# Kernel optimization log

Measured on AMD Instinct MI355X. Metric: run time of the kernel, lower is better.

Reference implementation:

```python
import jax, jax.numpy as jnp
import numpy as np

B, F, D, A = 1024, 33, 128, 128  # batch, num_fields, embed_dim, attn_size (A must equal gnn dim)

def setup_inputs() -> dict:
    key = jax.random.key(0)
    k1, k2, k3, k4 = jax.random.split(key, 4)
    gnn_feature = jax.random.normal(k1, (B, A), dtype=jnp.float32)
    x = jax.random.normal(k2, (B, F, D), dtype=jnp.float32)
    # attention Linear(embed_dim -> attn_size): weight (A, D), bias (A,)
    lim = 1.0 / np.sqrt(D)
    attn_W = jax.random.uniform(k3, (A, D), minval=-lim, maxval=lim, dtype=jnp.float32)
    attn_b = jax.random.uniform(k4, (A,), minval=-lim, maxval=lim, dtype=jnp.float32)
    return {"gnn_feature": gnn_feature, "x": x, "attn_W": attn_W, "attn_b": attn_b}

def reference(gnn_feature, x, attn_W, attn_b):
    num_fields = x.shape[1]
    row, col = np.triu_indices(num_fields, k=1)  # P = F*(F-1)/2 pairs
    inner = x[:, row] * x[:, col]                # [B, P, D]
    fm = jax.nn.relu(jnp.einsum('bpd,ad->bpa', inner, attn_W) + attn_b)  # [B, P, A]
    # bmm(gnn[b,1,A], fm[b,p,A,1]) -> dot product per pair, softmax over pairs
    scores = jnp.einsum('ba,bpa->bp', gnn_feature, fm)  # [B, P]
    attn = jax.nn.softmax(scores, axis=1)               # [B, P]
    attn_output = jnp.einsum('bp,bpd->bd', attn, inner) * 100.0  # [B, D]
    return jnp.concatenate([gnn_feature, attn_output], axis=1)   # [B, A+D]
```

## Files before the change

kernel.cpp:

```cpp
#include <hip/hip_runtime.h>

#define FN 33
#define DN 128
#define AN 128
#define PN 528
#define XS 136
#define TS 36

typedef __attribute__((ext_vector_type(8))) _Float16 half8;
typedef __attribute__((ext_vector_type(4))) float f32x4;
typedef __attribute__((ext_vector_type(4))) unsigned int u32x4;

__device__ __forceinline__ unsigned int pkrtz(float a, float b) {
  return __builtin_bit_cast(unsigned int, __builtin_amdgcn_cvt_pkrtz(a, b));
}

__device__ __forceinline__ float row_sum16(float v) {
  v += __builtin_bit_cast(float, __builtin_amdgcn_update_dpp(0, __builtin_bit_cast(int, v), 0x128, 0xF, 0xF, false));
  v += __builtin_bit_cast(float, __builtin_amdgcn_update_dpp(0, __builtin_bit_cast(int, v), 0x124, 0xF, 0xF, false));
  v += __builtin_bit_cast(float, __builtin_amdgcn_update_dpp(0, __builtin_bit_cast(int, v), 0x122, 0xF, 0xF, false));
  v += __builtin_bit_cast(float, __builtin_amdgcn_update_dpp(0, __builtin_bit_cast(int, v), 0x121, 0xF, 0xF, false));
  return v;
}

#define XLOAD(XV, XT, BB)                                                     \
  {                                                                           \
    const f32x4* xb = (const f32x4*)(xg + (size_t)(BB) * FN * DN);            \
    _Pragma("unroll")                                                         \
    for (int s = 0; s < 4; s++) {                                             \
      XV[s] = xb[tid + s * 256];                                              \
      asm volatile("" : "+v"(XV[s]));                                         \
    }                                                                         \
    if (tid < 32) XT = xb[1024 + tid];                                        \
    asm volatile("" : "+v"(XT));                                              \
  }

#define XSTORE(XV, XT, BUFI)                                                  \
  {                                                                           \
    _Pragma("unroll")                                                         \
    for (int s = 0; s < 4; s++) {                                             \
      const int idx = tid + s * 256;                                          \
      const int i = idx >> 5, d0 = (idx & 31) << 2;                           \
      *(uint2*)&xh[BUFI][i * XS + d0] =                                       \
          make_uint2(pkrtz(XV[s].x, XV[s].y), pkrtz(XV[s].z, XV[s].w));       \
    }                                                                         \
    if (tid < 32) {                                                           \
      const int idx = 1024 + tid;                                             \
      const int i = idx >> 5, d0 = (idx & 31) << 2;                           \
      *(uint2*)&xh[BUFI][i * XS + d0] =                                       \
          make_uint2(pkrtz(XT.x, XT.y), pkrtz(XT.z, XT.w));                   \
    }                                                                         \
  }

#define WALK(XHB, GB, SPB, RMAXP)                                             \
  {                                                                           \
    const int t_beg = mh ? 17 : 0;                                            \
    const int t_end = mh ? 33 : 17;                                           \
    float wm = -3.4e38f;                                                      \
    unsigned int rc_next = rowcol[t_beg * 16 + u];                            \
    for (int t = t_beg; t < t_end; ++t) {                                     \
      const unsigned int rc = rc_next;                                        \
      if (t + 1 < t_end) rc_next = rowcol[(t + 1) * 16 + u];                  \
      const int r = rc & 255, c = rc >> 8;                                    \
      const _Float16* xr_base = &XHB[r * XS + q * 8];                         \
      const _Float16* xc_base = &XHB[c * XS + q * 8];                         \
      f32x4 acc[4];                                                           \
      _Pragma("unroll")                                                       \
      for (int nn = 0; nn < 4; nn++)                                          \
        acc[nn] = (f32x4){barr[nn], barr[nn], barr[nn], barr[nn]};            \
      __builtin_amdgcn_s_setprio(1);                                          \
      _Pragma("unroll")                                                       \
      for (int kk = 0; kk < 4; kk++) {                                        \
        half8 af = *(const half8*)(xr_base + kk * 32) *                       \
                   *(const half8*)(xc_base + kk * 32);                        \
        _Pragma("unroll")                                                     \
        for (int nn = 0; nn < 4; nn++)                                        \
          acc[nn] = __builtin_amdgcn_mfma_f32_16x16x32_f16(af, Bf[nn][kk],    \
                                                           acc[nn], 0, 0, 0);  \
      }                                                                       \
      __builtin_amdgcn_s_setprio(0);                                          \
      float sc[4] = {0.f, 0.f, 0.f, 0.f};                                     \
      _Pragma("unroll")                                                       \
      for (int nn = 0; nn < 4; nn++)                                          \
        _Pragma("unroll")                                                     \
        for (int rr = 0; rr < 4; rr++)                                        \
          sc[rr] = fmaf(fmaxf(acc[nn][rr], 0.f), GB[nn], sc[rr]);             \
      _Pragma("unroll")                                                       \
      for (int rr = 0; rr < 4; rr++) sc[rr] = row_sum16(sc[rr]);              \
      wm = fmaxf(wm, fmaxf(fmaxf(sc[0], sc[1]), fmaxf(sc[2], sc[3])));        \
      if (u == 0)                                                             \
        *(f32x4*)&SPB[t * 16 + q * 4] = (f32x4){sc[0], sc[1], sc[2], sc[3]};  \
    }                                                                         \
    wm = fmaxf(wm, __shfl_xor(wm, 16, 64));                                   \
    wm = fmaxf(wm, __shfl_xor(wm, 32, 64));                                   \
    if (lane == 0) RMAXP[wave] = wm;                                          \
  }

#define SPH(PARM)                                                             \
  {                                                                           \
    const float Mh = fmaxf(rmax[PARM][0], rmax[PARM][2]) +                    \
                     fmaxf(rmax[PARM][1], rmax[PARM][3]);                     \
    float s0 = sp[PARM][0][tid] + sp[PARM][1][tid];                           \
    float s1 = sp[PARM][0][tid + 256] + sp[PARM][1][tid + 256];               \
    float e0 = __expf(s0 - Mh);                                               \
    float e1 = __expf(s1 - Mh);                                               \
    unsigned int rc = rowcol[tid];                                            \
    attn2d[PARM][(rc & 255) * TS + ((rc >> 8) - (rc & 255) - 1)] = e0;        \
    rc = rowcol[tid + 256];                                                   \
    attn2d[PARM][(rc & 255) * TS + ((rc >> 8) - (rc & 255) - 1)] = e1;        \
    float e2 = 0.f;                                                           \
    if (tid < 16) {                                                           \
      float s2 = sp[PARM][0][tid + 512] + sp[PARM][1][tid + 512];             \
      e2 = __expf(s2 - Mh);                                                   \
      rc = rowcol[tid + 512];                                                 \
      attn2d[PARM][(rc & 255) * TS + ((rc >> 8) - (rc & 255) - 1)] = e2;      \
    }                                                                         \
    float ls = (e0 + e1) + e2;                                                \
    _Pragma("unroll")                                                         \
    for (int off = 32; off >= 1; off >>= 1) ls += __shfl_xor(ls, off, 64);    \
    if (lane == 0) rsum[PARM][wave] = ls;                                     \
  }

#define EPH(PARM, XHB, BB)                                                    \
  if (tid < 128) {                                                            \
    const float Zb = (rsum[PARM][0] + rsum[PARM][1]) +                        \
                     (rsum[PARM][2] + rsum[PARM][3]);                         \
    const int d = tid;                                                        \
    float xcol[36];                                                           \
    _Pragma("unroll")                                                         \
    for (int i = 0; i < FN; i++) xcol[i] = (float)XHB[i * XS + d];            \
    xcol[33] = 0.f; xcol[34] = 0.f; xcol[35] = 0.f;                           \
    float accv = 0.f;                                                         \
    _Pragma("unroll")                                                         \
    for (int i = 0; i < 32; i++) {                                            \
      const int L = FN - 1 - i;                                               \
      const int nf4 = (L + 3) >> 2;                                           \
      float ti = 0.f;                                                         \
      _Pragma("unroll")                                                       \
      for (int t = 0; t < nf4; t++) {                                         \
        f32x4 a4 = *(const f32x4*)&attn2d[PARM][i * TS + t * 4];              \
        ti = fmaf(a4.x, xcol[i + 1 + t * 4 + 0], ti);                         \
        ti = fmaf(a4.y, xcol[i + 1 + t * 4 + 1], ti);                         \
        ti = fmaf(a4.z, xcol[i + 1 + t * 4 + 2], ti);                         \
        ti = fmaf(a4.w, xcol[i + 1 + t * 4 + 3], ti);                         \
      }                                                                       \
      accv = fmaf(xcol[i], ti, accv);                                         \
    }                                                                         \
    out[(size_t)(BB) * (AN + DN) + AN + d] = accv * (100.0f / Zb);            \
  } else {                                                                    \
    const int a = tid - 128;                                                  \
    out[(size_t)(BB) * (AN + DN) + a] = gnn[(size_t)(BB) * AN + a];           \
  }

__global__ __launch_bounds__(256, 2)
void afm_kernel(const float* __restrict__ gnn, const float* __restrict__ xg,
                const float* __restrict__ Wg,  const float* __restrict__ bg,
                float* __restrict__ out)
{
  __shared__ __align__(16) _Float16 xh[2][FN * XS];
  __shared__ __align__(16) float attn2d[2][FN * TS];
  __shared__ __align__(16) float sp[2][2][PN];
  __shared__ unsigned short rowcol[PN];
  __shared__ float rmax[2][4], rsum[2][4];

  const int tid  = threadIdx.x;
  const int b0   = blockIdx.x * 2;
  const int b1   = b0 + 1;
  const int wave = tid >> 6;
  const int lane = tid & 63;
  const int q    = lane >> 4;
  const int u    = lane & 15;
  const int nh   = wave & 1;
  const int mh   = wave >> 1;

  f32x4 xv0[4], xv1[4];
  f32x4 xt0 = {0,0,0,0}, xt1 = {0,0,0,0};
  XLOAD(xv0, xt0, b0);
  XLOAD(xv1, xt1, b1);

  half8 Bf[4][4];
  float g0[4], g1[4], barr[4];
  #pragma unroll
  for (int nn = 0; nn < 4; nn++) {
    const int a = nh * 64 + nn * 16 + u;
    const float* src = Wg + (size_t)a * DN + q * 8;
    #pragma unroll
    for (int kk = 0; kk < 4; kk++) {
      f32x4 w0 = *(const f32x4*)(src + kk * 32);
      f32x4 w1 = *(const f32x4*)(src + kk * 32 + 4);
      u32x4 pk;
      pk.x = pkrtz(w0.x, w0.y);
      pk.y = pkrtz(w0.z, w0.w);
      pk.z = pkrtz(w1.x, w1.y);
      pk.w = pkrtz(w1.z, w1.w);
      Bf[nn][kk] = __builtin_bit_cast(half8, pk);
      asm volatile("" : "+v"(Bf[nn][kk]));
    }
    g0[nn] = gnn[(size_t)b0 * AN + a];
    g1[nn] = gnn[(size_t)b1 * AN + a];
    barr[nn] = bg[a];
    asm volatile("" : "+v"(g0[nn]), "+v"(g1[nn]), "+v"(barr[nn]));
  }

  {
    float* a2z = &attn2d[0][0];
    for (int idx = tid; idx < 2 * FN * TS; idx += 256) a2z[idx] = 0.0f;
    for (int p = tid; p < PN; p += 256) {
      int i = 0, rem = p;
      while (rem >= FN - 1 - i) { rem -= FN - 1 - i; i++; }
      rowcol[p] = (unsigned short)(i | ((i + 1 + rem) << 8));
    }
  }
  XSTORE(xv0, xt0, 0);
  XSTORE(xv1, xt1, 1);
  __syncthreads();

  WALK(xh[0], g0, (&sp[0][nh][0]), rmax[0]);
  __syncthreads();

  SPH(0);
  WALK(xh[1], g1, (&sp[1][nh][0]), rmax[1]);
  __syncthreads();

  SPH(1);
  EPH(0, xh[0], b0);
  __syncthreads();

  EPH(1, xh[1], b1);
}

extern "C" void kernel_launch(void* const* d_in, const int* in_sizes, int n_in,
                              void* d_out, int out_size, void* d_ws, size_t ws_size,
                              hipStream_t stream) {
  (void)n_in; (void)out_size; (void)d_ws; (void)ws_size;
  const float* gnn  = (const float*)d_in[0];
  const float* x    = (const float*)d_in[1];
  const float* W    = (const float*)d_in[2];
  const float* bias = (const float*)d_in[3];
  float* out = (float*)d_out;
  const int Bn = in_sizes[0] / AN;
  afm_kernel<<<dim3(Bn / 2), dim3(256), 0, stream>>>(gnn, x, W, bias, out);
}
```

Baseline: 107.9 us.

## Transpose MFMA operands for cheaper score reduction and split epilogue across all threads

Swaps the MFMA operand order so each lane holds four attention outputs for one pair. The per-pair score reduction therefore becomes in-lane FMAs plus two cross-row shuffles instead of four DPP row sums, with bias and gnn loaded as vector quads. The epilogue weighted sum is now split across all 256 threads by row parity, with partial sums combined through shared memory, instead of leaving half the block idle. This adds shared storage and an extra barrier per batch element.

```diff
diff --git a/kernel.cpp b/kernel.cpp
--- a/kernel.cpp
+++ b/kernel.cpp
@@ -15,11 +15,11 @@
   return __builtin_bit_cast(unsigned int, __builtin_amdgcn_cvt_pkrtz(a, b));
 }
 
-__device__ __forceinline__ float row_sum16(float v) {
-  v += __builtin_bit_cast(float, __builtin_amdgcn_update_dpp(0, __builtin_bit_cast(int, v), 0x128, 0xF, 0xF, false));
-  v += __builtin_bit_cast(float, __builtin_amdgcn_update_dpp(0, __builtin_bit_cast(int, v), 0x124, 0xF, 0xF, false));
-  v += __builtin_bit_cast(float, __builtin_amdgcn_update_dpp(0, __builtin_bit_cast(int, v), 0x122, 0xF, 0xF, false));
-  v += __builtin_bit_cast(float, __builtin_amdgcn_update_dpp(0, __builtin_bit_cast(int, v), 0x121, 0xF, 0xF, false));
+__device__ __forceinline__ float row_max16(float v) {
+  v = fmaxf(v, __builtin_bit_cast(float, __builtin_amdgcn_update_dpp(0, __builtin_bit_cast(int, v), 0x128, 0xF, 0xF, false)));
+  v = fmaxf(v, __builtin_bit_cast(float, __builtin_amdgcn_update_dpp(0, __builtin_bit_cast(int, v), 0x124, 0xF, 0xF, false)));
+  v = fmaxf(v, __builtin_bit_cast(float, __builtin_amdgcn_update_dpp(0, __builtin_bit_cast(int, v), 0x122, 0xF, 0xF, false)));
+  v = fmaxf(v, __builtin_bit_cast(float, __builtin_amdgcn_update_dpp(0, __builtin_bit_cast(int, v), 0x121, 0xF, 0xF, false)));
   return v;
 }
 
@@ -52,7 +52,7 @@
     }                                                                         \
   }
 
-#define WALK(XHB, GB, SPB, RMAXP)                                             \
+#define WALK(XHB, GQ, SPB, RMAXP)                                             \
   {                                                                           \
     const int t_beg = mh ? 17 : 0;                                            \
     const int t_end = mh ? 33 : 17;                                           \
@@ -66,8 +66,7 @@
       const _Float16* xc_base = &XHB[c * XS + q * 8];                         \
       f32x4 acc[4];                                                           \
       _Pragma("unroll")                                                       \
-      for (int nn = 0; nn < 4; nn++)                                          \
-        acc[nn] = (f32x4){barr[nn], barr[nn], barr[nn], barr[nn]};            \
+      for (int nn = 0; nn < 4; nn++) acc[nn] = bq[nn];                        \
       __builtin_amdgcn_s_setprio(1);                                          \
       _Pragma("unroll")                                                       \
       for (int kk = 0; kk < 4; kk++) {                                        \
@@ -75,24 +74,34 @@
                    *(const half8*)(xc_base + kk * 32);                        \
         _Pragma("unroll")                                                     \
         for (int nn = 0; nn < 4; nn++)                                        \
-          acc[nn] = __builtin_amdgcn_mfma_f32_16x16x32_f16(af, Bf[nn][kk],    \
+          acc[nn] = __builtin_amdgcn_mfma_f32_16x16x32_f16(Bf[nn][kk], af,    \
                                                            acc[nn], 0, 0, 0);  \
       }                                                                       \
       __builtin_amdgcn_s_setprio(0);                                          \
-      float sc[4] = {0.f, 0.f, 0.f, 0.f};                                     \
-      _Pragma("unroll")                                                       \
-      for (int nn = 0; nn < 4; nn++)                                          \
-        _Pragma("unroll")                                                     \
-        for (int rr = 0; rr < 4; rr++)                                        \
-          sc[rr] = fmaf(fmaxf(acc[nn][rr], 0.f), GB[nn], sc[rr]);             \
-      _Pragma("unroll")                                                       \
-      for (int rr = 0; rr < 4; rr++) sc[rr] = row_sum16(sc[rr]);              \
-      wm = fmaxf(wm, fmaxf(fmaxf(sc[0], sc[1]), fmaxf(sc[2], sc[3])));        \
-      if (u == 0)                                                             \
-        *(f32x4*)&SPB[t * 16 + q * 4] = (f32x4){sc[0], sc[1], sc[2], sc[3]};  \
-    }                                                                         \
-    wm = fmaxf(wm, __shfl_xor(wm, 16, 64));                                   \
-    wm = fmaxf(wm, __shfl_xor(wm, 32, 64));                                   \
+      float sa0 = 0.f, sa1 = 0.f, sa2 = 0.f, sa3 = 0.f;                       \
+      sa0 = fmaf(fmaxf(acc[0][0], 0.f), GQ[0].x, sa0);                        \
+      sa0 = fmaf(fmaxf(acc[0][1], 0.f), GQ[0].y, sa0);                        \
+      sa0 = fmaf(fmaxf(acc[0][2], 0.f), GQ[0].z, sa0);                        \
+      sa0 = fmaf(fmaxf(acc[0][3], 0.f), GQ[0].w, sa0);                        \
+      sa1 = fmaf(fmaxf(acc[1][0], 0.f), GQ[1].x, sa1);                        \
+      sa1 = fmaf(fmaxf(acc[1][1], 0.f), GQ[1].y, sa1);                        \
+      sa1 = fmaf(fmaxf(acc[1][2], 0.f), GQ[1].z, sa1);                        \
+      sa1 = fmaf(fmaxf(acc[1][3], 0.f), GQ[1].w, sa1);                        \
+      sa2 = fmaf(fmaxf(acc[2][0], 0.f), GQ[2].x, sa2);                        \
+      sa2 = fmaf(fmaxf(acc[2][1], 0.f), GQ[2].y, sa2);                        \
+      sa2 = fmaf(fmaxf(acc[2][2], 0.f), GQ[2].z, sa2);                        \
+      sa2 = fmaf(fmaxf(acc[2][3], 0.f), GQ[2].w, sa2);                        \
+      sa3 = fmaf(fmaxf(acc[3][0], 0.f), GQ[3].x, sa3);                        \
+      sa3 = fmaf(fmaxf(acc[3][1], 0.f), GQ[3].y, sa3);                        \
+      sa3 = fmaf(fmaxf(acc[3][2], 0.f), GQ[3].z, sa3);                        \
+      sa3 = fmaf(fmaxf(acc[3][3], 0.f), GQ[3].w, sa3);                        \
+      float s = (sa0 + sa1) + (sa2 + sa3);                                    \
+      s += __shfl_xor(s, 16, 64);                                             \
+      s += __shfl_xor(s, 32, 64);                                             \
+      wm = fmaxf(wm, s);                                                      \
+      if (lane < 16) SPB[t * 16 + lane] = s;                                  \
+    }                                                                         \
+    wm = row_max16(wm);                                                       \
     if (lane == 0) RMAXP[wave] = wm;                                          \
   }
 
@@ -121,11 +130,10 @@
     if (lane == 0) rsum[PARM][wave] = ls;                                     \
   }
 
-#define EPH(PARM, XHB, BB)                                                    \
-  if (tid < 128) {                                                            \
-    const float Zb = (rsum[PARM][0] + rsum[PARM][1]) +                        \
-                     (rsum[PARM][2] + rsum[PARM][3]);                         \
-    const int d = tid;                                                        \
+#define EPI(PARM, XHB)                                                        \
+  {                                                                           \
+    const int d = tid & 127;                                                  \
+    const int h = tid >> 7;                                                   \
     float xcol[36];                                                           \
     _Pragma("unroll")                                                         \
     for (int i = 0; i < FN; i++) xcol[i] = (float)XHB[i * XS + d];            \
@@ -133,6 +141,7 @@
     float accv = 0.f;                                                         \
     _Pragma("unroll")                                                         \
     for (int i = 0; i < 32; i++) {                                            \
+      if ((i & 1) != h) continue;                                             \
       const int L = FN - 1 - i;                                               \
       const int nf4 = (L + 3) >> 2;                                           \
       float ti = 0.f;                                                         \
@@ -146,7 +155,15 @@
       }                                                                       \
       accv = fmaf(xcol[i], ti, accv);                                         \
     }                                                                         \
-    out[(size_t)(BB) * (AN + DN) + AN + d] = accv * (100.0f / Zb);            \
+    part[PARM][tid] = accv;                                                   \
+  }
+
+#define OUTW(PARM, BB)                                                        \
+  if (tid < 128) {                                                            \
+    const float Zb = (rsum[PARM][0] + rsum[PARM][1]) +                        \
+                     (rsum[PARM][2] + rsum[PARM][3]);                         \
+    float tot = part[PARM][tid] + part[PARM][tid + 128];                      \
+    out[(size_t)(BB) * (AN + DN) + AN + tid] = tot * (100.0f / Zb);           \
   } else {                                                                    \
     const int a = tid - 128;                                                  \
     out[(size_t)(BB) * (AN + DN) + a] = gnn[(size_t)(BB) * AN + a];           \
@@ -160,6 +177,7 @@
   __shared__ __align__(16) _Float16 xh[2][FN * XS];
   __shared__ __align__(16) float attn2d[2][FN * TS];
   __shared__ __align__(16) float sp[2][2][PN];
+  __shared__ __align__(16) float part[2][256];
   __shared__ unsigned short rowcol[PN];
   __shared__ float rmax[2][4], rsum[2][4];
 
@@ -179,7 +197,7 @@
   XLOAD(xv1, xt1, b1);
 
   half8 Bf[4][4];
-  float g0[4], g1[4], barr[4];
+  f32x4 bq[4], g0q[4], g1q[4];
   #pragma unroll
   for (int nn = 0; nn < 4; nn++) {
     const int a = nh * 64 + nn * 16 + u;
@@ -196,10 +214,11 @@
       Bf[nn][kk] = __builtin_bit_cast(half8, pk);
       asm volatile("" : "+v"(Bf[nn][kk]));
     }
-    g0[nn] = gnn[(size_t)b0 * AN + a];
-    g1[nn] = gnn[(size_t)b1 * AN + a];
-    barr[nn] = bg[a];
-    asm volatile("" : "+v"(g0[nn]), "+v"(g1[nn]), "+v"(barr[nn]));
+    const int abase = nh * 64 + nn * 16 + q * 4;
+    bq[nn]  = *(const f32x4*)&bg[abase];
+    g0q[nn] = *(const f32x4*)&gnn[(size_t)b0 * AN + abase];
+    g1q[nn] = *(const f32x4*)&gnn[(size_t)b1 * AN + abase];
+    asm volatile("" : "+v"(bq[nn]), "+v"(g0q[nn]), "+v"(g1q[nn]));
   }
 
   {
@@ -215,18 +234,22 @@
   XSTORE(xv1, xt1, 1);
   __syncthreads();
 
-  WALK(xh[0], g0, (&sp[0][nh][0]), rmax[0]);
+  WALK(xh[0], g0q, (&sp[0][nh][0]), rmax[0]);
   __syncthreads();
 
   SPH(0);
-  WALK(xh[1], g1, (&sp[1][nh][0]), rmax[1]);
+  WALK(xh[1], g1q, (&sp[1][nh][0]), rmax[1]);
   __syncthreads();
 
   SPH(1);
-  EPH(0, xh[0], b0);
-  __syncthreads();
-
-  EPH(1, xh[1], b1);
+  EPI(0, xh[0]);
+  __syncthreads();
+
+  OUTW(0, b0);
+  EPI(1, xh[1]);
+  __syncthreads();
+
+  OUTW(1, b1);
 }
 
 extern "C" void kernel_launch(void* const* d_in, const int* in_sizes, int n_in,
```

Measured after the change: 105.2 us. 2.5% less time.
